# Performance work log

Measured on AMD Instinct MI355X. Metric: run time of the kernel, lower is better.

## Reference

```python
import jax, jax.numpy as jnp
import numpy as np

B, S, D, H = 4, 2048, 1024, 16
HD = D // H  # 64


def setup_inputs() -> dict:
    key = jax.random.key(0)
    ks = jax.random.split(key, 12)
    s = 1.0 / np.sqrt(D)
    return {
        "q": jax.random.normal(ks[0], (B, S, D), jnp.float32),
        "k": jax.random.normal(ks[1], (B, S, D), jnp.float32),
        "v": jax.random.normal(ks[2], (B, S, D), jnp.float32),
        "mask": jnp.zeros((B, 1, 1, S), jnp.float32),
        "Wq": jax.random.normal(ks[3], (D, D), jnp.float32) * s,
        "bq": jnp.zeros((D,), jnp.float32),
        "Wk": jax.random.normal(ks[4], (D, D), jnp.float32) * s,
        "bk": jnp.zeros((D,), jnp.float32),
        "Wv": jax.random.normal(ks[5], (D, D), jnp.float32) * s,
        "bv": jnp.zeros((D,), jnp.float32),
        "Wo": jax.random.normal(ks[6], (D, D), jnp.float32) * s,
        "bo": jnp.zeros((D,), jnp.float32),
    }


def _split_heads(x):
    # [B, S, D] -> [B, H, S, HD]
    b, s, _ = x.shape
    return x.reshape(b, s, H, HD).transpose(0, 2, 1, 3)


def reference(q, k, v, mask, Wq, bq, Wk, bk, Wv, bv, Wo, bo):
    _q = _split_heads(q @ Wq + bq)
    _k = _split_heads(k @ Wk + bk)
    _v = _split_heads(v @ Wv + bv)
    # NOTE: original scales by (head_dim + 1e-8), NOT sqrt(head_dim)
    score = jnp.einsum("bhqd,bhkd->bhqk", _q, _k) / (HD + 1e-8)
    score = score + mask * (-1e9)
    attn = jax.nn.softmax(score, axis=-1)
    out = jnp.einsum("bhqk,bhkd->bhqd", attn, _v)  # [B, H, S, HD]
    out = out.transpose(0, 2, 1, 3).reshape(q.shape[0], q.shape[1], D)
    # dropout in inference mode -> identity
    return out @ Wo + bo
```

## Files before the change

### kernel.cpp

```cpp
#include <hip/hip_runtime.h>

#define DN 1024
#define SN 2048
#define BATCH 4
#define HN 16
#define HDN 64

typedef __attribute__((ext_vector_type(8))) short bf16x8;
typedef __attribute__((ext_vector_type(4))) float f32x4;
typedef __attribute__((ext_vector_type(16))) float f32x16;
typedef __attribute__((ext_vector_type(4))) unsigned int u32x4;

#define QSC 0.022542110013890054f
#define MSC -1.4426950408889634e9f

static __device__ __forceinline__ unsigned short f2b(float f) {
  unsigned u = __float_as_uint(f);
  unsigned r = (u + 0x7fffu + ((u >> 16) & 1u)) >> 16;
  return (unsigned short)r;
}

static __device__ __forceinline__ void gload16(const void* g, const void* l) {
  __builtin_amdgcn_global_load_lds(
      (const __attribute__((address_space(1))) unsigned int*)g,
      (__attribute__((address_space(3))) unsigned int*)l, 16, 0, 0);
}

static __device__ __forceinline__ unsigned cvtpk(float lo, float hi) {
  unsigned w;
  asm volatile("v_cvt_pk_bf16_f32 %0, %1, %2" : "=v"(w) : "v"(lo), "v"(hi));
  return w;
}

static __device__ __forceinline__ float vsum16(const f32x16& v) {
  float a0 = v[0] + v[1], a1 = v[2] + v[3];
  float a2 = v[4] + v[5], a3 = v[6] + v[7];
  float a4 = v[8] + v[9], a5 = v[10] + v[11];
  float a6 = v[12] + v[13], a7 = v[14] + v[15];
  float b0 = a0 + a1, b1 = a2 + a3, b2 = a4 + a5, b3 = a6 + a7;
  return (b0 + b1) + (b2 + b3);
}

__global__ void wtrans(const float* __restrict__ W0, const float* __restrict__ W1,
                       const float* __restrict__ W2, const float* __restrict__ W3,
                       unsigned short* __restrict__ Wt) {
  __shared__ float tile[32][33];
  const int z = blockIdx.z;
  const float* W = (z == 0) ? W0 : (z == 1) ? W1 : (z == 2) ? W2 : W3;
  const int tx = threadIdx.x, ty = threadIdx.y;
  const int n0 = blockIdx.x * 32, k0 = blockIdx.y * 32;
#pragma unroll
  for (int j = ty; j < 32; j += 8)
    tile[j][tx] = W[(long)(k0 + j) * DN + n0 + tx];
  __syncthreads();
  unsigned short* o = Wt + (long)z * DN * DN;
#pragma unroll
  for (int j = ty; j < 32; j += 8)
    o[(long)(n0 + j) * DN + k0 + tx] = f2b(tile[tx][j]);
}

__global__ __launch_bounds__(256, 3) void gemm_qkv(
    const float* __restrict__ q, const float* __restrict__ k, const float* __restrict__ v,
    const unsigned short* __restrict__ Wt,
    const float* __restrict__ bq, const float* __restrict__ bk, const float* __restrict__ bv,
    unsigned short* __restrict__ Qh, unsigned short* __restrict__ Kh,
    unsigned short* __restrict__ Vh) {
  const int z = blockIdx.z;
  const float* A = (z == 0) ? q : (z == 1) ? k : v;
  const unsigned short* Bt = Wt + (size_t)z * DN * DN;
  const float* bias = (z == 0) ? bq : (z == 1) ? bk : bv;

  __shared__ float As[2][128 * 32];
  __shared__ unsigned short Bs[2][128 * 32];
  const int t = threadIdx.x;
  const int lane = t & 63, w = t >> 6;
  const int rl = lane & 15, g = lane >> 4;
  const int wm = (w >> 1) << 6, wn = (w & 1) << 6;
  const long bm = (long)blockIdx.x * 128, bn = (long)blockIdx.y * 128;
  const int K = DN;

  f32x4 acc[4][4] = {};

#define QSTAGE(buf, kk)                                                          \
  {                                                                              \
    _Pragma("unroll") for (int i_ = 0; i_ < 4; ++i_) {                           \
      int c_ = i_ * 256 + t;                                                     \
      int r_ = c_ >> 3, sl_ = c_ & 7;                                            \
      gload16(A + (bm + r_) * K + (kk) + ((sl_ ^ (r_ & 7)) << 2),                \
              &As[buf][(i_ * 256 + (w << 6)) * 4]);                              \
    }                                                                            \
    _Pragma("unroll") for (int i_ = 0; i_ < 2; ++i_) {                           \
      int c_ = i_ * 256 + t;                                                     \
      int r_ = c_ >> 2, sl_ = c_ & 3;                                            \
      gload16(Bt + (bn + r_) * K + (kk) + sl_ * 8,                               \
              &Bs[buf][(i_ * 256 + (w << 6)) * 8]);                              \
    }                                                                            \
  }

  QSTAGE(0, 0);
  asm volatile("s_waitcnt vmcnt(0)" ::: "memory");
  __syncthreads();

  for (int ks = 0; ks < K / 32; ++ks) {
    const int cur = ks & 1;
    if (ks + 1 < K / 32) QSTAGE(cur ^ 1, (ks + 1) * 32);

    bf16x8 af[4], bfr[4];
#pragma unroll
    for (int mf = 0; mf < 4; ++mf) {
      int r_ = wm + mf * 16 + rl;
      const float* Ar = As[cur] + r_ * 32;
      f32x4 lo = *(const f32x4*)(Ar + (((2 * g) ^ (r_ & 7)) << 2));
      f32x4 hi = *(const f32x4*)(Ar + (((2 * g + 1) ^ (r_ & 7)) << 2));
      u32x4 uw = {cvtpk(lo[0], lo[1]), cvtpk(lo[2], lo[3]),
                  cvtpk(hi[0], hi[1]), cvtpk(hi[2], hi[3])};
      af[mf] = __builtin_bit_cast(bf16x8, uw);
    }
#pragma unroll
    for (int nf = 0; nf < 4; ++nf)
      bfr[nf] = *(const bf16x8*)(&Bs[cur][(wn + nf * 16 + rl) * 32 + g * 8]);
#pragma unroll
    for (int mf = 0; mf < 4; ++mf)
#pragma unroll
      for (int nf = 0; nf < 4; ++nf)
        acc[mf][nf] = __builtin_amdgcn_mfma_f32_16x16x32_bf16(af[mf], bfr[nf], acc[mf][nf], 0, 0, 0);

    asm volatile("s_waitcnt vmcnt(0)" ::: "memory");
    __syncthreads();
  }
#undef QSTAGE

  const float scale = (z == 0) ? QSC : 1.0f;
#pragma unroll
  for (int mf = 0; mf < 4; ++mf)
#pragma unroll
    for (int nf = 0; nf < 4; ++nf) {
      long col = bn + wn + nf * 16 + rl;
      float bv2 = bias[col];
      if (z == 2) {
        long row0 = bm + wm + mf * 16 + g * 4;
        long bb = row0 >> 11, ss = row0 & 2047;
        ushort4 pack;
        pack.x = f2b(acc[mf][nf][0] + bv2);
        pack.y = f2b(acc[mf][nf][1] + bv2);
        pack.z = f2b(acc[mf][nf][2] + bv2);
        pack.w = f2b(acc[mf][nf][3] + bv2);
        *(ushort4*)(Vh + (bb * DN + col) * SN + ss) = pack;
      } else {
        unsigned short* Cout = (z == 0) ? Qh : Kh;
#pragma unroll
        for (int r = 0; r < 4; ++r) {
          long row = bm + wm + mf * 16 + g * 4 + r;
          Cout[row * DN + col] = f2b((acc[mf][nf][r] + bv2) * scale);
        }
      }
    }
}

__global__ __launch_bounds__(256, 4) void gemm_out(
    const unsigned short* __restrict__ A, const unsigned short* __restrict__ Bt,
    const float* __restrict__ bias, float* __restrict__ Cout) {
  __shared__ unsigned short Asm2[2][128 * 32];
  __shared__ unsigned short Bsm[2][128 * 32];
  const int t = threadIdx.x;
  const int lane = t & 63, w = t >> 6;
  const int rl = lane & 15, g = lane >> 4;
  const int wm = (w >> 1) << 6, wn = (w & 1) << 6;
  const long bm = (long)blockIdx.x * 128, bn = (long)blockIdx.y * 128;
  const int K = DN, N = DN;

  f32x4 acc[4][4] = {};
  const int c0 = t, c1 = 256 + t;
  const int r0 = c0 >> 2, s0i = c0 & 3;
  const int r1 = c1 >> 2, s1i = c1 & 3;

#define OSTAGE(buf, kk)                                                     \
  {                                                                         \
    gload16(A + (bm + r0) * K + (kk) + s0i * 8, &Asm2[buf][(w << 6) * 8]);  \
    gload16(A + (bm + r1) * K + (kk) + s1i * 8, &Asm2[buf][(256 + (w << 6)) * 8]); \
    gload16(Bt + (bn + r0) * K + (kk) + s0i * 8, &Bsm[buf][(w << 6) * 8]);  \
    gload16(Bt + (bn + r1) * K + (kk) + s1i * 8, &Bsm[buf][(256 + (w << 6)) * 8]); \
  }

  OSTAGE(0, 0);
  asm volatile("s_waitcnt vmcnt(0)" ::: "memory");
  __syncthreads();

  for (int ks = 0; ks < K / 32; ++ks) {
    const int cur = ks & 1;
    if (ks + 1 < K / 32) OSTAGE(cur ^ 1, (ks + 1) * 32);
    bf16x8 af[4], bfr[4];
#pragma unroll
    for (int mf = 0; mf < 4; ++mf)
      af[mf] = *(const bf16x8*)(&Asm2[cur][(wm + mf * 16 + rl) * 32 + g * 8]);
#pragma unroll
    for (int nf = 0; nf < 4; ++nf)
      bfr[nf] = *(const bf16x8*)(&Bsm[cur][(wn + nf * 16 + rl) * 32 + g * 8]);
#pragma unroll
    for (int mf = 0; mf < 4; ++mf)
#pragma unroll
      for (int nf = 0; nf < 4; ++nf)
        acc[mf][nf] = __builtin_amdgcn_mfma_f32_16x16x32_bf16(af[mf], bfr[nf], acc[mf][nf], 0, 0, 0);
    asm volatile("s_waitcnt vmcnt(0)" ::: "memory");
    __syncthreads();
  }
#undef OSTAGE

#pragma unroll
  for (int mf = 0; mf < 4; ++mf)
#pragma unroll
    for (int nf = 0; nf < 4; ++nf) {
      long col = bn + wn + nf * 16 + rl;
      float bv2 = bias[col];
#pragma unroll
      for (int r = 0; r < 4; ++r) {
        long row = bm + wm + mf * 16 + g * 4 + r;
        Cout[row * N + col] = acc[mf][nf][r] + bv2;
      }
    }
}

__global__ __launch_bounds__(256, 4) void attnk(
    const unsigned short* __restrict__ Qh, const unsigned short* __restrict__ Kh,
    const unsigned short* __restrict__ Vt, const float* __restrict__ mask,
    unsigned short* __restrict__ AO) {
  const int t = threadIdx.x, lane = t & 63, w = t >> 6;
  const int ql = lane & 31, hi = lane >> 5;
  const int qb = blockIdx.x * 128;
  const int h = blockIdx.y, b = blockIdx.z;

  __shared__ unsigned short KV[2][8192];
  __shared__ float ms[SN];

  const unsigned short* Kp = Kh + (long)b * SN * DN + h * HDN;
  const unsigned short* Vp = Vt + ((long)b * DN + h * HDN) * SN;

  {
    const float4* mp = (const float4*)(mask + (long)b * SN);
    float4* md = (float4*)ms;
    float4 v0 = mp[t], v1 = mp[256 + t];
    v0.x *= MSC; v0.y *= MSC; v0.z *= MSC; v0.w *= MSC;
    v1.x *= MSC; v1.y *= MSC; v1.z *= MSC; v1.w *= MSC;
    md[t] = v0;
    md[256 + t] = v1;
  }

#define STAGE(buf, tt)                                                          \
  {                                                                             \
    const int base_ = (tt) * 64;                                                \
    _Pragma("unroll") for (int i_ = 0; i_ < 2; ++i_) {                          \
      int c_ = i_ * 256 + t;                                                    \
      int r_ = c_ >> 3, sl_ = c_ & 7;                                           \
      gload16(Kp + (long)(base_ + r_) * DN + ((sl_ ^ (r_ & 7)) << 3),           \
              &KV[buf][(i_ * 256 + (w << 6)) * 8]);                             \
      gload16(Vp + (long)r_ * SN + base_ + ((sl_ ^ (r_ & 7)) << 3),             \
              &KV[buf][4096 + (i_ * 256 + (w << 6)) * 8]);                      \
    }                                                                           \
  }

  STAGE(0, 0);

  const unsigned short* Qp = Qh + ((long)b * SN + qb + (w << 5) + ql) * DN + h * HDN;
  bf16x8 qf[4];
#pragma unroll
  for (int f = 0; f < 4; ++f)
    qf[f] = *(const bf16x8*)(Qp + f * 16 + hi * 8);

  asm volatile("s_waitcnt vmcnt(0)" ::: "memory");
  __syncthreads();

  unsigned mflags;
  {
    int mt = lane & 31;
    const f32x4* mrow = (const f32x4*)(ms + mt * 64);
    bool nz = false;
#pragma unroll
    for (int i2 = 0; i2 < 16; ++i2) {
      f32x4 mv2 = mrow[i2];
      nz = nz || (mv2[0] != 0.f) || (mv2[1] != 0.f) || (mv2[2] != 0.f) || (mv2[3] != 0.f);
    }
    unsigned long long bal = __ballot(nz);
    mflags = (unsigned)bal | (unsigned)(bal >> 32);
  }

  f32x16 O[2] = {};
  float l_run = 0.f;

  for (int tt = 0; tt < SN / 64; ++tt) {
    const int cur = tt & 1;
    if (tt < SN / 64 - 1) STAGE(cur ^ 1, tt + 1);
    const unsigned short* Kb = &KV[cur][0];
    const unsigned short* Vb = &KV[cur][4096];

    f32x16 s0, s1;
    if ((mflags >> tt) & 1u) {
#pragma unroll
      for (int j = 0; j < 4; ++j) {
        f32x4 m0 = *(const f32x4*)(ms + tt * 64 + 8 * j + 4 * hi);
        f32x4 m1 = *(const f32x4*)(ms + tt * 64 + 32 + 8 * j + 4 * hi);
#pragma unroll
        for (int i2 = 0; i2 < 4; ++i2) {
          s0[4 * j + i2] = m0[i2];
          s1[4 * j + i2] = m1[i2];
        }
      }
    } else {
#pragma unroll
      for (int r = 0; r < 16; ++r) { s0[r] = 0.f; s1[r] = 0.f; }
    }

    __builtin_amdgcn_s_setprio(1);
#pragma unroll
    for (int f = 0; f < 4; ++f) {
      bf16x8 a0 = *(const bf16x8*)(Kb + ql * 64 + (((f * 2 + hi) ^ (ql & 7)) << 3));
      bf16x8 a1 = *(const bf16x8*)(Kb + (32 + ql) * 64 + (((f * 2 + hi) ^ (ql & 7)) << 3));
      s0 = __builtin_amdgcn_mfma_f32_32x32x16_bf16(a0, qf[f], s0, 0, 0, 0);
      s1 = __builtin_amdgcn_mfma_f32_32x32x16_bf16(a1, qf[f], s1, 0, 0, 0);
    }
    __builtin_amdgcn_s_setprio(0);

#pragma unroll
    for (int r = 0; r < 16; ++r) {
      s0[r] = __builtin_amdgcn_exp2f(s0[r]);
      s1[r] = __builtin_amdgcn_exp2f(s1[r]);
    }
    float rs = vsum16(s0) + vsum16(s1);
    rs += __shfl_xor(rs, 32);
    l_run += rs;

    unsigned aw[8], bw[8];
#pragma unroll
    for (int j = 0; j < 4; ++j) {
      aw[j]     = cvtpk(s0[4 * j], s0[4 * j + 1]);
      bw[j]     = cvtpk(s0[4 * j + 2], s0[4 * j + 3]);
      aw[4 + j] = cvtpk(s1[4 * j], s1[4 * j + 1]);
      bw[4 + j] = cvtpk(s1[4 * j + 2], s1[4 * j + 3]);
    }
    bf16x8 pb[4];
#pragma unroll
    for (int ks = 0; ks < 4; ++ks) {
      unsigned x0 = aw[2 * ks], y0 = aw[2 * ks + 1];
      unsigned x1 = bw[2 * ks], y1 = bw[2 * ks + 1];
      asm volatile("v_permlane32_swap_b32 %0, %1" : "+v"(x0), "+v"(y0));
      asm volatile("v_permlane32_swap_b32 %0, %1" : "+v"(x1), "+v"(y1));
      u32x4 wv = {x0, x1, y0, y1};
      pb[ks] = __builtin_bit_cast(bf16x8, wv);
    }

    __builtin_amdgcn_s_setprio(1);
#pragma unroll
    for (int ks = 0; ks < 4; ++ks)
#pragma unroll
      for (int da = 0; da < 2; ++da) {
        const int dr = da * 32 + ql;
        bf16x8 va = *(const bf16x8*)(Vb + dr * 64 + (((ks * 2 + hi) ^ (dr & 7)) << 3));
        O[da] = __builtin_amdgcn_mfma_f32_32x32x16_bf16(va, pb[ks], O[da], 0, 0, 0);
      }
    __builtin_amdgcn_s_setprio(0);

    asm volatile("s_waitcnt vmcnt(0)" ::: "memory");
    __syncthreads();
  }
#undef STAGE

  float inv = 1.0f / l_run;
  unsigned short* dst = AO + ((long)b * SN + qb + (w << 5) + ql) * DN + h * HDN;
#pragma unroll
  for (int da = 0; da < 2; ++da)
#pragma unroll
    for (int j = 0; j < 4; ++j) {
      ushort4 pk;
      pk.x = f2b(O[da][4 * j + 0] * inv);
      pk.y = f2b(O[da][4 * j + 1] * inv);
      pk.z = f2b(O[da][4 * j + 2] * inv);
      pk.w = f2b(O[da][4 * j + 3] * inv);
      *(ushort4*)(dst + da * 32 + 8 * j + 4 * hi) = pk;
    }
}

extern "C" void kernel_launch(void* const* d_in, const int* in_sizes, int n_in,
                              void* d_out, int out_size, void* d_ws, size_t ws_size,
                              hipStream_t stream) {
  (void)in_sizes; (void)n_in; (void)out_size; (void)ws_size;
  const float* q    = (const float*)d_in[0];
  const float* k    = (const float*)d_in[1];
  const float* v    = (const float*)d_in[2];
  const float* mask = (const float*)d_in[3];
  const float* Wq   = (const float*)d_in[4];
  const float* bq   = (const float*)d_in[5];
  const float* Wk   = (const float*)d_in[6];
  const float* bk   = (const float*)d_in[7];
  const float* Wv   = (const float*)d_in[8];
  const float* bv   = (const float*)d_in[9];
  const float* Wo   = (const float*)d_in[10];
  const float* bo   = (const float*)d_in[11];

  char* ws = (char*)d_ws;
  unsigned short* AO = (unsigned short*)ws;
  unsigned short* Wt = (unsigned short*)(ws + (size_t)16777216);
  unsigned short* Qh = (unsigned short*)(ws + (size_t)16777216 + 8388608);
  unsigned short* Kh = Qh + (size_t)8192 * 1024;
  unsigned short* Vh = Kh + (size_t)8192 * 1024;

  wtrans<<<dim3(32, 32, 4), dim3(32, 8), 0, stream>>>(Wq, Wk, Wv, Wo, Wt);

  gemm_qkv<<<dim3(64, 8, 3), 256, 0, stream>>>(q, k, v, Wt, bq, bk, bv, Qh, Kh, Vh);

  attnk<<<dim3(16, 16, 4), 256, 0, stream>>>(Qh, Kh, Vh, mask, AO);

  gemm_out<<<dim3(64, 8), 256, 0, stream>>>(AO, Wt + (size_t)3 * 1024 * 1024, bo,
                                            (float*)d_out);
}
```

Before: 371.2 us.

## Triple-buffer GEMM LDS stages with partial vmcnt waits in projection kernels

Both projection GEMMs move from double to triple buffering of LDS tiles. Loads run two k-steps ahead, and each iteration waits with a partial s_waitcnt vmcnt so the newest stage stays in flight while the current one is consumed. The goal is to hide global-to-LDS load latency behind MFMA work instead of draining all loads every iteration. In exchange, LDS use rises and the occupancy hints drop (3 to 2, 4 to 3), and correctness now depends on the hand-counted vmcnt values matching the number of issued loads.

Measured after the change: 386.8 us. 4.2% more time.

```diff
diff --git a/kernel.cpp b/kernel.cpp
--- a/kernel.cpp
+++ b/kernel.cpp
@@ -59,7 +59,7 @@
     o[(long)(n0 + j) * DN + k0 + tx] = f2b(tile[tx][j]);
 }
 
-__global__ __launch_bounds__(256, 3) void gemm_qkv(
+__global__ __launch_bounds__(256, 2) void gemm_qkv(
     const float* __restrict__ q, const float* __restrict__ k, const float* __restrict__ v,
     const unsigned short* __restrict__ Wt,
     const float* __restrict__ bq, const float* __restrict__ bk, const float* __restrict__ bv,
@@ -70,14 +70,14 @@
   const unsigned short* Bt = Wt + (size_t)z * DN * DN;
   const float* bias = (z == 0) ? bq : (z == 1) ? bk : bv;
 
-  __shared__ float As[2][128 * 32];
-  __shared__ unsigned short Bs[2][128 * 32];
+  __shared__ float As[3][128 * 32];
+  __shared__ unsigned short Bs[3][128 * 32];
   const int t = threadIdx.x;
   const int lane = t & 63, w = t >> 6;
   const int rl = lane & 15, g = lane >> 4;
   const int wm = (w >> 1) << 6, wn = (w & 1) << 6;
   const long bm = (long)blockIdx.x * 128, bn = (long)blockIdx.y * 128;
-  const int K = DN;
+  const int K = DN, NK = DN / 32;
 
   f32x4 acc[4][4] = {};
 
@@ -98,12 +98,15 @@
   }
 
   QSTAGE(0, 0);
-  asm volatile("s_waitcnt vmcnt(0)" ::: "memory");
-  __syncthreads();
-
-  for (int ks = 0; ks < K / 32; ++ks) {
-    const int cur = ks & 1;
-    if (ks + 1 < K / 32) QSTAGE(cur ^ 1, (ks + 1) * 32);
+  QSTAGE(1, 32);
+
+  for (int ks = 0; ks < NK; ++ks) {
+    const int cur = ks % 3;
+    if (ks + 2 < NK) QSTAGE((ks + 2) % 3, (ks + 2) * 32);
+    if (ks + 2 < NK)      asm volatile("s_waitcnt vmcnt(12)" ::: "memory");
+    else if (ks + 1 < NK) asm volatile("s_waitcnt vmcnt(6)" ::: "memory");
+    else                  asm volatile("s_waitcnt vmcnt(0)" ::: "memory");
+    __builtin_amdgcn_s_barrier();
 
     bf16x8 af[4], bfr[4];
 #pragma unroll
@@ -125,8 +128,7 @@
       for (int nf = 0; nf < 4; ++nf)
         acc[mf][nf] = __builtin_amdgcn_mfma_f32_16x16x32_bf16(af[mf], bfr[nf], acc[mf][nf], 0, 0, 0);
 
-    asm volatile("s_waitcnt vmcnt(0)" ::: "memory");
-    __syncthreads();
+    __builtin_amdgcn_s_barrier();
   }
 #undef QSTAGE
 
@@ -157,17 +159,17 @@
     }
 }
 
-__global__ __launch_bounds__(256, 4) void gemm_out(
+__global__ __launch_bounds__(256, 3) void gemm_out(
     const unsigned short* __restrict__ A, const unsigned short* __restrict__ Bt,
     const float* __restrict__ bias, float* __restrict__ Cout) {
-  __shared__ unsigned short Asm2[2][128 * 32];
-  __shared__ unsigned short Bsm[2][128 * 32];
+  __shared__ unsigned short Asm2[3][128 * 32];
+  __shared__ unsigned short Bsm[3][128 * 32];
   const int t = threadIdx.x;
   const int lane = t & 63, w = t >> 6;
   const int rl = lane & 15, g = lane >> 4;
   const int wm = (w >> 1) << 6, wn = (w & 1) << 6;
   const long bm = (long)blockIdx.x * 128, bn = (long)blockIdx.y * 128;
-  const int K = DN, N = DN;
+  const int K = DN, N = DN, NK = DN / 32;
 
   f32x4 acc[4][4] = {};
   const int c0 = t, c1 = 256 + t;
@@ -183,12 +185,16 @@
   }
 
   OSTAGE(0, 0);
-  asm volatile("s_waitcnt vmcnt(0)" ::: "memory");
-  __syncthreads();
-
-  for (int ks = 0; ks < K / 32; ++ks) {
-    const int cur = ks & 1;
-    if (ks + 1 < K / 32) OSTAGE(cur ^ 1, (ks + 1) * 32);
+  OSTAGE(1, 32);
+
+  for (int ks = 0; ks < NK; ++ks) {
+    const int cur = ks % 3;
+    if (ks + 2 < NK) OSTAGE((ks + 2) % 3, (ks + 2) * 32);
+    if (ks + 2 < NK)      asm volatile("s_waitcnt vmcnt(8)" ::: "memory");
+    else if (ks + 1 < NK) asm volatile("s_waitcnt vmcnt(4)" ::: "memory");
+    else                  asm volatile("s_waitcnt vmcnt(0)" ::: "memory");
+    __builtin_amdgcn_s_barrier();
+
     bf16x8 af[4], bfr[4];
 #pragma unroll
     for (int mf = 0; mf < 4; ++mf)
@@ -201,8 +207,8 @@
 #pragma unroll
       for (int nf = 0; nf < 4; ++nf)
         acc[mf][nf] = __builtin_amdgcn_mfma_f32_16x16x32_bf16(af[mf], bfr[nf], acc[mf][nf], 0, 0, 0);
-    asm volatile("s_waitcnt vmcnt(0)" ::: "memory");
-    __syncthreads();
+
+    __builtin_amdgcn_s_barrier();
   }
 #undef OSTAGE
 
```

## Pre-convert QKV inputs to bf16 and compute softmax row sums via MFMA

Applied to the files above, without the earlier changes.

Adds a separate conversion pass that casts q/k/v from fp32 to bf16 into workspace, then runs a pure-bf16 QKV GEMM with halved A-tile traffic and no per-iteration conversion, when the workspace is large enough. If it is not, the fp32-input GEMM is still used. In attention, the per-row exp sum is computed by an extra MFMA against a ones vector instead of scalar adds and a shuffle. The trade is an extra pass over 100MB of input plus one more MFMA per k-step, and the row sum now comes from bf16-rounded probabilities.

Result: faster. 353.5 us (-4.8%).

```diff
diff --git a/kernel.cpp b/kernel.cpp
--- a/kernel.cpp
+++ b/kernel.cpp
@@ -30,15 +30,6 @@
   unsigned w;
   asm volatile("v_cvt_pk_bf16_f32 %0, %1, %2" : "=v"(w) : "v"(lo), "v"(hi));
   return w;
-}
-
-static __device__ __forceinline__ float vsum16(const f32x16& v) {
-  float a0 = v[0] + v[1], a1 = v[2] + v[3];
-  float a2 = v[4] + v[5], a3 = v[6] + v[7];
-  float a4 = v[8] + v[9], a5 = v[10] + v[11];
-  float a6 = v[12] + v[13], a7 = v[14] + v[15];
-  float b0 = a0 + a1, b1 = a2 + a3, b2 = a4 + a5, b3 = a6 + a7;
-  return (b0 + b1) + (b2 + b3);
 }
 
 __global__ void wtrans(const float* __restrict__ W0, const float* __restrict__ W1,
@@ -59,7 +50,104 @@
     o[(long)(n0 + j) * DN + k0 + tx] = f2b(tile[tx][j]);
 }
 
-__global__ __launch_bounds__(256, 3) void gemm_qkv(
+__global__ void cvt3(const float* __restrict__ q, const float* __restrict__ k,
+                     const float* __restrict__ v, unsigned short* __restrict__ Xb3) {
+  const int z = blockIdx.y;
+  const float* x = (z == 0) ? q : (z == 1) ? k : v;
+  const float4* xv = (const float4*)x;
+  ushort4* yv = (ushort4*)(Xb3 + (size_t)z * 8388608);
+  for (int i = blockIdx.x * 256 + threadIdx.x; i < (8388608 / 4); i += 2048 * 256) {
+    float4 vv = xv[i];
+    ushort4 o;
+    o.x = f2b(vv.x); o.y = f2b(vv.y); o.z = f2b(vv.z); o.w = f2b(vv.w);
+    yv[i] = o;
+  }
+}
+
+__global__ __launch_bounds__(256, 4) void gemm_qkv_b(
+    const unsigned short* __restrict__ Xb3, const unsigned short* __restrict__ Wt,
+    const float* __restrict__ bq, const float* __restrict__ bk, const float* __restrict__ bv,
+    unsigned short* __restrict__ Qh, unsigned short* __restrict__ Kh,
+    unsigned short* __restrict__ Vh) {
+  const int z = blockIdx.z;
+  const unsigned short* A = Xb3 + (size_t)z * 8388608;
+  const unsigned short* Bt = Wt + (size_t)z * DN * DN;
+  const float* bias = (z == 0) ? bq : (z == 1) ? bk : bv;
+
+  __shared__ unsigned short Asm2[2][128 * 32];
+  __shared__ unsigned short Bsm[2][128 * 32];
+  const int t = threadIdx.x;
+  const int lane = t & 63, w = t >> 6;
+  const int rl = lane & 15, g = lane >> 4;
+  const int wm = (w >> 1) << 6, wn = (w & 1) << 6;
+  const long bm = (long)blockIdx.x * 128, bn = (long)blockIdx.y * 128;
+  const int K = DN;
+
+  f32x4 acc[4][4] = {};
+  const int c0 = t, c1 = 256 + t;
+  const int r0 = c0 >> 2, s0i = c0 & 3;
+  const int r1 = c1 >> 2, s1i = c1 & 3;
+
+#define BSTAGE(buf, kk)                                                     \
+  {                                                                         \
+    gload16(A + (bm + r0) * K + (kk) + s0i * 8, &Asm2[buf][(w << 6) * 8]);  \
+    gload16(A + (bm + r1) * K + (kk) + s1i * 8, &Asm2[buf][(256 + (w << 6)) * 8]); \
+    gload16(Bt + (bn + r0) * K + (kk) + s0i * 8, &Bsm[buf][(w << 6) * 8]);  \
+    gload16(Bt + (bn + r1) * K + (kk) + s1i * 8, &Bsm[buf][(256 + (w << 6)) * 8]); \
+  }
+
+  BSTAGE(0, 0);
+  asm volatile("s_waitcnt vmcnt(0)" ::: "memory");
+  __syncthreads();
+
+  for (int ks = 0; ks < K / 32; ++ks) {
+    const int cur = ks & 1;
+    if (ks + 1 < K / 32) BSTAGE(cur ^ 1, (ks + 1) * 32);
+    bf16x8 af[4], bfr[4];
+#pragma unroll
+    for (int mf = 0; mf < 4; ++mf)
+      af[mf] = *(const bf16x8*)(&Asm2[cur][(wm + mf * 16 + rl) * 32 + g * 8]);
+#pragma unroll
+    for (int nf = 0; nf < 4; ++nf)
+      bfr[nf] = *(const bf16x8*)(&Bsm[cur][(wn + nf * 16 + rl) * 32 + g * 8]);
+#pragma unroll
+    for (int mf = 0; mf < 4; ++mf)
+#pragma unroll
+      for (int nf = 0; nf < 4; ++nf)
+        acc[mf][nf] = __builtin_amdgcn_mfma_f32_16x16x32_bf16(af[mf], bfr[nf], acc[mf][nf], 0, 0, 0);
+    asm volatile("s_waitcnt vmcnt(0)" ::: "memory");
+    __syncthreads();
+  }
+#undef BSTAGE
+
+  const float scale = (z == 0) ? QSC : 1.0f;
+#pragma unroll
+  for (int mf = 0; mf < 4; ++mf)
+#pragma unroll
+    for (int nf = 0; nf < 4; ++nf) {
+      long col = bn + wn + nf * 16 + rl;
+      float bv2 = bias[col];
+      if (z == 2) {
+        long row0 = bm + wm + mf * 16 + g * 4;
+        long bb = row0 >> 11, ss = row0 & 2047;
+        ushort4 pack;
+        pack.x = f2b(acc[mf][nf][0] + bv2);
+        pack.y = f2b(acc[mf][nf][1] + bv2);
+        pack.z = f2b(acc[mf][nf][2] + bv2);
+        pack.w = f2b(acc[mf][nf][3] + bv2);
+        *(ushort4*)(Vh + (bb * DN + col) * SN + ss) = pack;
+      } else {
+        unsigned short* Cout = (z == 0) ? Qh : Kh;
+#pragma unroll
+        for (int r = 0; r < 4; ++r) {
+          long row = bm + wm + mf * 16 + g * 4 + r;
+          Cout[row * DN + col] = f2b((acc[mf][nf][r] + bv2) * scale);
+        }
+      }
+    }
+}
+
+__global__ __launch_bounds__(256, 3) void gemm_qkv_f(
     const float* __restrict__ q, const float* __restrict__ k, const float* __restrict__ v,
     const unsigned short* __restrict__ Wt,
     const float* __restrict__ bq, const float* __restrict__ bk, const float* __restrict__ bv,
@@ -104,7 +192,6 @@
   for (int ks = 0; ks < K / 32; ++ks) {
     const int cur = ks & 1;
     if (ks + 1 < K / 32) QSTAGE(cur ^ 1, (ks + 1) * 32);
-
     bf16x8 af[4], bfr[4];
 #pragma unroll
     for (int mf = 0; mf < 4; ++mf) {
@@ -124,7 +211,6 @@
 #pragma unroll
       for (int nf = 0; nf < 4; ++nf)
         acc[mf][nf] = __builtin_amdgcn_mfma_f32_16x16x32_bf16(af[mf], bfr[nf], acc[mf][nf], 0, 0, 0);
-
     asm volatile("s_waitcnt vmcnt(0)" ::: "memory");
     __syncthreads();
   }
@@ -283,8 +369,11 @@
     mflags = (unsigned)bal | (unsigned)(bal >> 32);
   }
 
+  const u32x4 onesw = {0x3F803F80u, 0x3F803F80u, 0x3F803F80u, 0x3F803F80u};
+  const bf16x8 vones = __builtin_bit_cast(bf16x8, onesw);
+
   f32x16 O[2] = {};
-  float l_run = 0.f;
+  f32x16 lacc = {};
 
   for (int tt = 0; tt < SN / 64; ++tt) {
     const int cur = tt & 1;
@@ -324,9 +413,6 @@
       s0[r] = __builtin_amdgcn_exp2f(s0[r]);
       s1[r] = __builtin_amdgcn_exp2f(s1[r]);
     }
-    float rs = vsum16(s0) + vsum16(s1);
-    rs += __shfl_xor(rs, 32);
-    l_run += rs;
 
     unsigned aw[8], bw[8];
 #pragma unroll
@@ -349,13 +435,15 @@
 
     __builtin_amdgcn_s_setprio(1);
 #pragma unroll
-    for (int ks = 0; ks < 4; ++ks)
+    for (int ks = 0; ks < 4; ++ks) {
 #pragma unroll
       for (int da = 0; da < 2; ++da) {
         const int dr = da * 32 + ql;
         bf16x8 va = *(const bf16x8*)(Vb + dr * 64 + (((ks * 2 + hi) ^ (dr & 7)) << 3));
         O[da] = __builtin_amdgcn_mfma_f32_32x32x16_bf16(va, pb[ks], O[da], 0, 0, 0);
       }
+      lacc = __builtin_amdgcn_mfma_f32_32x32x16_bf16(vones, pb[ks], lacc, 0, 0, 0);
+    }
     __builtin_amdgcn_s_setprio(0);
 
     asm volatile("s_waitcnt vmcnt(0)" ::: "memory");
@@ -363,7 +451,7 @@
   }
 #undef STAGE
 
-  float inv = 1.0f / l_run;
+  float inv = 1.0f / lacc[0];
   unsigned short* dst = AO + ((long)b * SN + qb + (w << 5) + ql) * DN + h * HDN;
 #pragma unroll
   for (int da = 0; da < 2; ++da)
@@ -381,7 +469,7 @@
 extern "C" void kernel_launch(void* const* d_in, const int* in_sizes, int n_in,
                               void* d_out, int out_size, void* d_ws, size_t ws_size,
                               hipStream_t stream) {
-  (void)in_sizes; (void)n_in; (void)out_size; (void)ws_size;
+  (void)in_sizes; (void)n_in; (void)out_size;
   const float* q    = (const float*)d_in[0];
   const float* k    = (const float*)d_in[1];
   const float* v    = (const float*)d_in[2];
@@ -396,15 +484,21 @@
   const float* bo   = (const float*)d_in[11];
 
   char* ws = (char*)d_ws;
-  unsigned short* AO = (unsigned short*)ws;
-  unsigned short* Wt = (unsigned short*)(ws + (size_t)16777216);
-  unsigned short* Qh = (unsigned short*)(ws + (size_t)16777216 + 8388608);
-  unsigned short* Kh = Qh + (size_t)8192 * 1024;
-  unsigned short* Vh = Kh + (size_t)8192 * 1024;
+  unsigned short* AO  = (unsigned short*)ws;
+  unsigned short* Wt  = (unsigned short*)(ws + (size_t)16777216);
+  unsigned short* Qh  = (unsigned short*)(ws + (size_t)16777216 + 8388608);
+  unsigned short* Kh  = Qh + (size_t)8192 * 1024;
+  unsigned short* Vh  = Kh + (size_t)8192 * 1024;
+  unsigned short* Xb3 = (unsigned short*)(ws + (size_t)75497472);
 
   wtrans<<<dim3(32, 32, 4), dim3(32, 8), 0, stream>>>(Wq, Wk, Wv, Wo, Wt);
 
-  gemm_qkv<<<dim3(64, 8, 3), 256, 0, stream>>>(q, k, v, Wt, bq, bk, bv, Qh, Kh, Vh);
+  if (ws_size >= (size_t)125829120) {
+    cvt3<<<dim3(2048, 3), 256, 0, stream>>>(q, k, v, Xb3);
+    gemm_qkv_b<<<dim3(64, 8, 3), 256, 0, stream>>>(Xb3, Wt, bq, bk, bv, Qh, Kh, Vh);
+  } else {
+    gemm_qkv_f<<<dim3(64, 8, 3), 256, 0, stream>>>(q, k, v, Wt, bq, bk, bv, Qh, Kh, Vh);
+  }
 
   attnk<<<dim3(16, 16, 4), 256, 0, stream>>>(Qh, Kh, Vh, mask, AO);
 
```
